# Kernel optimization log

Hardware: AMD Instinct MI355X
Metric: run time of the kernel (lower is better)

## Reference

```python
import jax, jax.numpy as jnp
import numpy as np

B, N, C, H = 8, 4096, 256, 8
D = C // H
HID = 4 * C
EPS = 1e-5

def _ln(x, w, b):
    mu = jnp.mean(x, axis=-1, keepdims=True)
    var = jnp.var(x, axis=-1, keepdims=True)
    return (x - mu) * jax.lax.rsqrt(var + EPS) * w + b

def setup_inputs() -> dict:
    key = jax.random.key(0)
    ks = jax.random.split(key, 16)
    s = lambda k, shp, scale=0.02: jax.random.normal(k, shp, dtype=jnp.float32) * scale
    return {
        "input_": jax.random.normal(ks[0], (B, N, C), dtype=jnp.float32),
        "prev_state": jax.random.normal(ks[1], (B, N, C), dtype=jnp.float32),
        "pos_embed": jax.random.normal(ks[2], (1, N, C), dtype=jnp.float32),
        "norm1_w": jnp.ones((C,), jnp.float32), "norm1_b": jnp.zeros((C,), jnp.float32),
        "norm2_w": jnp.ones((C,), jnp.float32), "norm2_b": jnp.zeros((C,), jnp.float32),
        "norm3_w": jnp.ones((C,), jnp.float32), "norm3_b": jnp.zeros((C,), jnp.float32),
        "qkv_input_w": s(ks[3], (3 * C, C)),
        "qkv_state_w": s(ks[4], (3 * C, C)),
        "proj_w": s(ks[5], (C, C)), "proj_b": jnp.zeros((C,), jnp.float32),
        "gate_w": s(ks[6], (C, 2 * C)), "gate_b": jnp.zeros((C,), jnp.float32),
        "fc1_w": s(ks[7], (HID, C)), "fc1_b": jnp.zeros((HID,), jnp.float32),
        "fc2_w": s(ks[8], (C, HID)), "fc2_b": jnp.zeros((C,), jnp.float32),
    }

def reference(input_, prev_state, pos_embed,
              norm1_w, norm1_b, norm2_w, norm2_b, norm3_w, norm3_b,
              qkv_input_w, qkv_state_w, proj_w, proj_b,
              gate_w, gate_b, fc1_w, fc1_b, fc2_w, fc2_b):
    input_pos = input_ + pos_embed
    x_ln = _ln(input_pos, norm1_w, norm1_b)
    s_ln = _ln(prev_state, norm2_w, norm2_b)
    # fused QKV from input and state; torch Linear: x @ W.T
    qkv_i = (x_ln @ qkv_input_w.T).reshape(B, N, 3, H, D).transpose(2, 0, 3, 1, 4)
    qkv_s = (s_ln @ qkv_state_w.T).reshape(B, N, 3, H, D).transpose(2, 0, 3, 1, 4)
    q = qkv_i[0] + qkv_s[0]  # [B,H,N,D]
    k = qkv_i[1] + qkv_s[1]
    v = qkv_i[2] + qkv_s[2]
    phi_q = jax.nn.elu(q) + 1.0
    phi_k = jax.nn.elu(k) + 1.0
    # (phi_q @ phi_k^T) @ v reordered associatively to O(N*D^2)
    kv = jnp.einsum('bhnd,bhne->bhde', phi_k, v)        # [B,H,D,D]
    attn = jnp.einsum('bhnd,bhde->bhne', phi_q, kv)     # [B,H,N,D]
    attn = attn.transpose(0, 2, 1, 3).reshape(B, N, C)
    attn = attn @ proj_w.T + proj_b
    output = input_pos + attn
    stacked = jnp.concatenate([input_, prev_state], axis=2)
    update = jax.nn.sigmoid(stacked @ gate_w.T + gate_b)
    new_state = prev_state * (1.0 - update) + attn * update
    h = _ln(output, norm3_w, norm3_b)
    h = jax.nn.gelu(h @ fc1_w.T + fc1_b, approximate=False) @ fc2_w.T + fc2_b
    output = output + h
    return (output, new_state)
```

## Files before the change

kernel.cpp:

```cpp
#include <hip/hip_runtime.h>
#include <cmath>

typedef unsigned short u16;
typedef __attribute__((ext_vector_type(8))) short short8;
typedef __attribute__((ext_vector_type(4))) float f32x4;
typedef __attribute__((ext_vector_type(4))) u16 u16x4;

__device__ __forceinline__ float b2f(u16 u) {
    unsigned x = ((unsigned)u) << 16;
    return __builtin_bit_cast(float, x);
}
__device__ __forceinline__ u16 f2b(float f) {
    unsigned x = __builtin_bit_cast(unsigned, f);
    unsigned r = (x + 0x7fffu + ((x >> 16) & 1u)) >> 16;
    return (u16)r;
}
__device__ __forceinline__ float loadx(const void* p, size_t i, int f32) {
    return f32 ? ((const float*)p)[i] : b2f(((const u16*)p)[i]);
}
__device__ __forceinline__ void gl_lds16(const void* g, void* l) {
    __builtin_amdgcn_global_load_lds(
        (const __attribute__((address_space(1))) void*)g,
        (__attribute__((address_space(3))) void*)l, 16, 0, 0);
}
__device__ __forceinline__ float gelu_f(float x) {
    float y = 0.7978845608028654f * (x + 0.044715f * x * x * x);
    float e = __expf(2.f * y);
    float t = 1.f - 2.f / (e + 1.f);
    return 0.5f * x * (1.f + t);
}

#define BB 8
#define NN 4096
#define CC 256
#define HH 8
#define DD 32
#define HID 1024
#define MTOK (BB*NN)
#define TOKEL ((size_t)MTOK*CC)
#define TOKELC 8388608

#define WS_INPUT_POS 0u
#define WS_PHIQ   16777216u
#define WS_PHIK   33554432u
#define WS_V      50331648u
#define WS_XLN    67108864u
#define WS_SLN    83886080u
#define WS_OUTPRE 100663296u
#define WS_FLAG   117440512u

#define OFF_QKVI  0u
#define OFF_QKVS  196608u
#define OFF_PROJW 393216u
#define OFF_GATEW 458752u
#define OFF_FC1W  589824u
#define OFF_FC2W  851968u
#define OFF_PROJB 1114112u
#define OFF_GATEB 1114368u
#define OFF_FC1B  1114624u
#define OFF_FC2B  1115648u
#define WTOT      1115904u

__device__ __attribute__((aligned(16))) u16 g_wb[WTOT];
__device__ __attribute__((aligned(16))) u16 g_inb[TOKELC];
__device__ __attribute__((aligned(16))) u16 g_prevb[TOKELC];
__device__ __attribute__((aligned(16))) u16 g_ugate[TOKELC];

__global__ __launch_bounds__(64) void detect_kernel(const u16* __restrict__ in0,
                                                    int* __restrict__ flag)
{
    int t = threadIdx.x;
    u16 w = in0[2 * t];
    int e = (w >> 7) & 0xFF;
    int bad = (e < 64 || e > 192) ? 1 : 0;
    unsigned long long m = __ballot(bad);
    if (t == 0) *flag = (__popcll(m) > 8) ? 1 : 0;
}

__global__ __launch_bounds__(256) void wconv_kernel(
    const void* qkvi, const void* qkvs, const void* projw, const void* gatew,
    const void* fc1w, const void* fc2w, const void* projb, const void* gateb,
    const void* fc1b, const void* fc2b, const int* __restrict__ flagp)
{
    const int f32 = *flagp;
    unsigned i = blockIdx.x * 256 + threadIdx.x;
    if (i >= WTOT) return;
    const void* src; unsigned off;
    if      (i < OFF_QKVS)  { src = qkvi;  off = OFF_QKVI; }
    else if (i < OFF_PROJW) { src = qkvs;  off = OFF_QKVS; }
    else if (i < OFF_GATEW) { src = projw; off = OFF_PROJW; }
    else if (i < OFF_FC1W)  { src = gatew; off = OFF_GATEW; }
    else if (i < OFF_FC2W)  { src = fc1w;  off = OFF_FC1W; }
    else if (i < OFF_PROJB) { src = fc2w;  off = OFF_FC2W; }
    else if (i < OFF_GATEB) { src = projb; off = OFF_PROJB; }
    else if (i < OFF_FC1B)  { src = gateb; off = OFF_GATEB; }
    else if (i < OFF_FC2B)  { src = fc1b;  off = OFF_FC1B; }
    else                    { src = fc2b;  off = OFF_FC2B; }
    g_wb[i] = f2b(loadx(src, i - off, f32));
}

__global__ __launch_bounds__(256) void prep_kernel(
    const void* __restrict__ inp, const void* __restrict__ prev,
    const void* __restrict__ pos,
    const void* __restrict__ w1, const void* __restrict__ b1,
    const void* __restrict__ w2, const void* __restrict__ b2,
    u16* __restrict__ input_pos, u16* __restrict__ x_ln, u16* __restrict__ s_ln,
    const int* __restrict__ flagp)
{
    const int f32 = *flagp;
    const int m = blockIdx.x * 4 + (threadIdx.x >> 6);
    const int lane = threadIdx.x & 63;
    const int e0 = lane * 4;
    const int n = m & (NN - 1);
    const size_t idx = (size_t)m * CC + e0;

    float inr[4], ip[4];
    if (f32) {
        f32x4 a = *(const f32x4*)((const float*)inp + idx);
        f32x4 p = *(const f32x4*)((const float*)pos + (size_t)n * CC + e0);
        #pragma unroll
        for (int r = 0; r < 4; ++r) { inr[r] = a[r]; ip[r] = a[r] + p[r]; }
    } else {
        u16x4 a = *(const u16x4*)((const u16*)inp + idx);
        u16x4 p = *(const u16x4*)((const u16*)pos + (size_t)n * CC + e0);
        #pragma unroll
        for (int r = 0; r < 4; ++r) { inr[r] = b2f(a[r]); ip[r] = inr[r] + b2f(p[r]); }
    }
    {
        u16x4 gi;
        #pragma unroll
        for (int r = 0; r < 4; ++r) gi[r] = f2b(inr[r]);
        *(u16x4*)(g_inb + idx) = gi;
    }
    float s = 0.f, s2 = 0.f;
    #pragma unroll
    for (int r = 0; r < 4; ++r) { s += ip[r]; s2 += ip[r] * ip[r]; }
    #pragma unroll
    for (int o = 1; o < 64; o <<= 1) { s += __shfl_xor(s, o, 64); s2 += __shfl_xor(s2, o, 64); }
    float mu = s * (1.f / 256.f);
    float rs = rsqrtf(s2 * (1.f / 256.f) - mu * mu + 1e-5f);
    float wv[4], bv[4];
    if (f32) {
        f32x4 w4 = *(const f32x4*)((const float*)w1 + e0);
        f32x4 b4 = *(const f32x4*)((const float*)b1 + e0);
        #pragma unroll
        for (int r = 0; r < 4; ++r) { wv[r] = w4[r]; bv[r] = b4[r]; }
    } else {
        u16x4 w4 = *(const u16x4*)((const u16*)w1 + e0);
        u16x4 b4 = *(const u16x4*)((const u16*)b1 + e0);
        #pragma unroll
        for (int r = 0; r < 4; ++r) { wv[r] = b2f(w4[r]); bv[r] = b2f(b4[r]); }
    }
    {
        u16x4 ipo, xo;
        #pragma unroll
        for (int r = 0; r < 4; ++r) {
            ipo[r] = f2b(ip[r]);
            xo[r]  = f2b((ip[r] - mu) * rs * wv[r] + bv[r]);
        }
        *(u16x4*)(input_pos + idx) = ipo;
        *(u16x4*)(x_ln + idx) = xo;
    }

    float pv[4];
    if (f32) {
        f32x4 a = *(const f32x4*)((const float*)prev + idx);
        #pragma unroll
        for (int r = 0; r < 4; ++r) pv[r] = a[r];
    } else {
        u16x4 a = *(const u16x4*)((const u16*)prev + idx);
        #pragma unroll
        for (int r = 0; r < 4; ++r) pv[r] = b2f(a[r]);
    }
    {
        u16x4 gp;
        #pragma unroll
        for (int r = 0; r < 4; ++r) gp[r] = f2b(pv[r]);
        *(u16x4*)(g_prevb + idx) = gp;
    }
    s = 0.f; s2 = 0.f;
    #pragma unroll
    for (int r = 0; r < 4; ++r) { s += pv[r]; s2 += pv[r] * pv[r]; }
    #pragma unroll
    for (int o = 1; o < 64; o <<= 1) { s += __shfl_xor(s, o, 64); s2 += __shfl_xor(s2, o, 64); }
    mu = s * (1.f / 256.f);
    rs = rsqrtf(s2 * (1.f / 256.f) - mu * mu + 1e-5f);
    if (f32) {
        f32x4 w4 = *(const f32x4*)((const float*)w2 + e0);
        f32x4 b4 = *(const f32x4*)((const float*)b2 + e0);
        #pragma unroll
        for (int r = 0; r < 4; ++r) { wv[r] = w4[r]; bv[r] = b4[r]; }
    } else {
        u16x4 w4 = *(const u16x4*)((const u16*)w2 + e0);
        u16x4 b4 = *(const u16x4*)((const u16*)b2 + e0);
        #pragma unroll
        for (int r = 0; r < 4; ++r) { wv[r] = b2f(w4[r]); bv[r] = b2f(b4[r]); }
    }
    {
        u16x4 so;
        #pragma unroll
        for (int r = 0; r < 4; ++r) so[r] = f2b((pv[r] - mu) * rs * wv[r] + bv[r]);
        *(u16x4*)(s_ln + idx) = so;
    }
}

__global__ __launch_bounds__(256) void ln3_blend_kernel(
    const u16* __restrict__ op, const void* __restrict__ w,
    const void* __restrict__ b, u16* __restrict__ out,
    const u16* __restrict__ ap, const void* __restrict__ prevraw,
    void* __restrict__ dout, const int* __restrict__ flagp)
{
    const int f32 = *flagp;
    const int m = blockIdx.x * 4 + (threadIdx.x >> 6);
    const int lane = threadIdx.x & 63;
    const int e0 = lane * 4;
    const size_t idx = (size_t)m * CC + e0;

    u16x4 x4 = *(const u16x4*)(op + idx);
    float x[4];
    #pragma unroll
    for (int r = 0; r < 4; ++r) x[r] = b2f(x4[r]);
    float s = 0.f, s2 = 0.f;
    #pragma unroll
    for (int r = 0; r < 4; ++r) { s += x[r]; s2 += x[r] * x[r]; }
    #pragma unroll
    for (int o = 1; o < 64; o <<= 1) { s += __shfl_xor(s, o, 64); s2 += __shfl_xor(s2, o, 64); }
    float mu = s * (1.f / 256.f);
    float rs = rsqrtf(s2 * (1.f / 256.f) - mu * mu + 1e-5f);
    float wv[4], bv[4];
    if (f32) {
        f32x4 w4 = *(const f32x4*)((const float*)w + e0);
        f32x4 b4 = *(const f32x4*)((const float*)b + e0);
        #pragma unroll
        for (int r = 0; r < 4; ++r) { wv[r] = w4[r]; bv[r] = b4[r]; }
    } else {
        u16x4 w4 = *(const u16x4*)((const u16*)w + e0);
        u16x4 b4 = *(const u16x4*)((const u16*)b + e0);
        #pragma unroll
        for (int r = 0; r < 4; ++r) { wv[r] = b2f(w4[r]); bv[r] = b2f(b4[r]); }
    }
    {
        u16x4 o4;
        #pragma unroll
        for (int r = 0; r < 4; ++r) o4[r] = f2b((x[r] - mu) * rs * wv[r] + bv[r]);
        *(u16x4*)(out + idx) = o4;
    }

    u16x4 a4 = *(const u16x4*)(ap + idx);
    u16x4 u4 = *(const u16x4*)(g_ugate + idx);
    if (f32) {
        f32x4 pv = *(const f32x4*)((const float*)prevraw + idx);
        f32x4 o;
        #pragma unroll
        for (int r = 0; r < 4; ++r) {
            float u = b2f(u4[r]);
            o[r] = pv[r] * (1.f - u) + b2f(a4[r]) * u;
        }
        *(f32x4*)((float*)dout + TOKEL + idx) = o;
    } else {
        u16x4 pv = *(const u16x4*)((const u16*)prevraw + idx);
        u16x4 o;
        #pragma unroll
        for (int r = 0; r < 4; ++r) {
            float u = b2f(u4[r]);
            o[r] = f2b(b2f(pv[r]) * (1.f - u) + b2f(a4[r]) * u);
        }
        *(u16x4*)((u16*)dout + TOKEL + idx) = o;
    }
}

__global__ __launch_bounds__(64) void kv_mfma(
    const u16* __restrict__ phik_t, const u16* __restrict__ v_t,
    float* __restrict__ kvout)
{
    const int bh = blockIdx.x;
    const int k0 = blockIdx.y * 256;
    const int lane = threadIdx.x;
    const int quad = lane >> 4, lr = lane & 15;

    const u16* A = phik_t + (size_t)bh * DD * NN;
    const u16* W = v_t    + (size_t)bh * DD * NN;

    f32x4 acc[2][2];
    #pragma unroll
    for (int i = 0; i < 2; ++i)
        #pragma unroll
        for (int j = 0; j < 2; ++j) { f32x4 z = {0.f,0.f,0.f,0.f}; acc[i][j] = z; }

    for (int kk = k0; kk < k0 + 256; kk += 32) {
        short8 a0 = *(const short8*)(A + (size_t)lr * NN + kk + quad * 8);
        short8 a1 = *(const short8*)(A + (size_t)(16 + lr) * NN + kk + quad * 8);
        short8 w0 = *(const short8*)(W + (size_t)lr * NN + kk + quad * 8);
        short8 w1 = *(const short8*)(W + (size_t)(16 + lr) * NN + kk + quad * 8);
        acc[0][0] = __builtin_amdgcn_mfma_f32_16x16x32_bf16(a0, w0, acc[0][0], 0, 0, 0);
        acc[0][1] = __builtin_amdgcn_mfma_f32_16x16x32_bf16(a0, w1, acc[0][1], 0, 0, 0);
        acc[1][0] = __builtin_amdgcn_mfma_f32_16x16x32_bf16(a1, w0, acc[1][0], 0, 0, 0);
        acc[1][1] = __builtin_amdgcn_mfma_f32_16x16x32_bf16(a1, w1, acc[1][1], 0, 0, 0);
    }
    float* base = kvout + (size_t)bh * (DD * DD);
    #pragma unroll
    for (int i = 0; i < 2; ++i)
        #pragma unroll
        for (int j = 0; j < 2; ++j)
            #pragma unroll
            for (int r = 0; r < 4; ++r)
                atomicAdd(base + (i * 16 + quad * 4 + r) * DD + j * 16 + lr, acc[i][j][r]);
}

__global__ __launch_bounds__(256) void attn_mfma(
    const u16* __restrict__ phiq, const float* __restrict__ kv,
    u16* __restrict__ attn_tok)
{
    const int bh = blockIdx.x;
    const int b = bh >> 3, h = bh & 7;
    const int wv = threadIdx.x >> 6, lane = threadIdx.x & 63;
    const int quad = lane >> 4, lr = lane & 15;

    const float* kvb = kv + (size_t)bh * (DD * DD);
    short8 bf0, bf1;
    #pragma unroll
    for (int j = 0; j < 8; ++j) {
        int d = quad * 8 + j;
        bf0[j] = (short)f2b(kvb[d * DD + lr]);
        bf1[j] = (short)f2b(kvb[d * DD + 16 + lr]);
    }

    const u16* qb = phiq + (size_t)bh * NN * DD;
    const int n0 = blockIdx.y * 512 + wv * 128;
    #pragma unroll
    for (int t = 0; t < 8; ++t) {
        const int nt = n0 + t * 16;
        short8 af = *(const short8*)(qb + (size_t)(nt + lr) * DD + quad * 8);
        f32x4 c0 = {0.f,0.f,0.f,0.f}, c1 = {0.f,0.f,0.f,0.f};
        c0 = __builtin_amdgcn_mfma_f32_16x16x32_bf16(af, bf0, c0, 0, 0, 0);
        c1 = __builtin_amdgcn_mfma_f32_16x16x32_bf16(af, bf1, c1, 0, 0, 0);
        size_t base = ((size_t)b * NN + nt + quad * 4) * CC + h * DD;
        #pragma unroll
        for (int r = 0; r < 4; ++r) {
            attn_tok[base + (size_t)r * CC + lr]      = f2b(c0[r]);
            attn_tok[base + (size_t)r * CC + 16 + lr] = f2b(c1[r]);
        }
    }
}

#define BM 128
#define BN 128
#define BK 32

template <int MODE>
__global__ __launch_bounds__(256) void gemm_bt(
    const u16* __restrict__ A1in, const u16* __restrict__ A2in,
    int lda, int ldw, int K, int Ksplit, int wcol2,
    u16* __restrict__ o0, u16* __restrict__ o1,
    const u16* __restrict__ xa, const void* __restrict__ xr,
    void* __restrict__ oraw, const int* __restrict__ flagp)
{
    __shared__ __attribute__((aligned(16))) u16 ash[3][BM * BK];
    __shared__ __attribute__((aligned(16))) u16 bsh[3][BN * BK];

    const int f32 = (MODE == 4) ? *flagp : 0;

    const u16* W1; const u16* W2; const u16* bias = nullptr;
    if (MODE == 0)      { W1 = g_wb + OFF_QKVI; W2 = g_wb + OFF_QKVS; }
    else if (MODE == 1) { W1 = W2 = g_wb + OFF_PROJW; bias = g_wb + OFF_PROJB; }
    else if (MODE == 3) { W1 = W2 = g_wb + OFF_FC1W;  bias = g_wb + OFF_FC1B; }
    else                { W1 = W2 = g_wb + OFF_FC2W;  bias = g_wb + OFF_FC2B; }

    const int gx = gridDim.x;
    const int nwg = gx * (int)gridDim.y;
    const int hw = blockIdx.y * gx + blockIdx.x;
    const int qq = nwg >> 3, rr = nwg & 7;
    const int xc = hw & 7, pp = hw >> 3;
    const int nid = (xc < rr ? xc * (qq + 1) : rr * (qq + 1) + (xc - rr) * qq) + pp;
    const int bx = nid % gx, by = nid / gx;

    const bool isGate = (MODE == 1) && (bx >= 2);
    const bool swp = (MODE == 0) ? (bx < 2) : true;

    const int tid = threadIdx.x;
    const int lane = tid & 63;
    const int wv = tid >> 6;
    const int wm = wv >> 1, wn = wv & 1;
    const int quad = lane >> 4, lr = lane & 15;

    f32x4 acc[4][4];
    #pragma unroll
    for (int i = 0; i < 4; ++i)
        #pragma unroll
        for (int j = 0; j < 4; ++j) { f32x4 z = {0.f,0.f,0.f,0.f}; acc[i][j] = z; }

    const size_t arow0 = (size_t)by * BM;
    const int nbase_blk = isGate ? (bx - 2) * BN : bx * BN;
    const int ldw_eff = isGate ? 2 * CC : ldw;
    const int Keff = isGate ? 2 * CC : K;

    const int srow = lane & 31;
    const int sg   = (lane >> 5) << 3;
    const size_t aoff = (arow0 + wv * 32 + srow) * (size_t)lda + sg;
    const size_t woff = ((size_t)nbase_blk + wv * 32 + srow) * (size_t)ldw_eff + sg;

    auto stage = [&](int buf, int k0) {
        const u16* As; const u16* Ws; int ka, kw;
        if (isGate) {
            As = (k0 < CC) ? g_inb : g_prevb; ka = k0 & (CC - 1);
            Ws = g_wb + OFF_GATEW; kw = k0;
        } else if (MODE == 0) {
            if (k0 < Ksplit) { As = A1in; Ws = W1; ka = k0;          kw = k0; }
            else             { As = A2in; Ws = W2; ka = k0 - Ksplit; kw = k0 - Ksplit; }
        } else {
            As = A1in; Ws = W1; ka = k0; kw = k0;
        }
        const u16* ga = As + aoff + ka;
        u16* la = ash[buf] + (wv << 10);
        gl_lds16(ga, la);
        gl_lds16(ga + 16, la + 512);
        const u16* gw = Ws + woff + kw;
        u16* lb = bsh[buf] + (wv << 10);
        gl_lds16(gw, lb);
        gl_lds16(gw + 16, lb + 512);
    };

    auto compute = [&](int buf) {
        short8 af[4], bf[4];
        #pragma unroll
        for (int i = 0; i < 4; ++i) {
            const int ra = wm * 64 + i * 16 + lr;
            af[i] = *(const short8*)(ash[buf] + ((ra >> 5) << 10) + (quad << 8) + ((ra & 31) << 3));
        }
        #pragma unroll
        for (int j = 0; j < 4; ++j) {
            const int rb = wn * 64 + j * 16 + lr;
            bf[j] = *(const short8*)(bsh[buf] + ((rb >> 5) << 10) + (quad << 8) + ((rb & 31) << 3));
        }
        if (swp) {
            #pragma unroll
            for (int i = 0; i < 4; ++i)
                #pragma unroll
                for (int j = 0; j < 4; ++j)
                    acc[i][j] = __builtin_amdgcn_mfma_f32_16x16x32_bf16(bf[j], af[i], acc[i][j], 0, 0, 0);
        } else {
            #pragma unroll
            for (int i = 0; i < 4; ++i)
                #pragma unroll
                for (int j = 0; j < 4; ++j)
                    acc[i][j] = __builtin_amdgcn_mfma_f32_16x16x32_bf16(af[i], bf[j], acc[i][j], 0, 0, 0);
        }
    };

    const int NT = Keff / BK;
    stage(0, 0);
    stage(1, BK);
    for (int t = 0; t < NT; ++t) {
        if (t + 2 < NT) {
            stage((t + 2) % 3, (t + 2) * BK);
            asm volatile("s_waitcnt vmcnt(8)" ::: "memory");
        } else if (t + 1 < NT) {
            asm volatile("s_waitcnt vmcnt(4)" ::: "memory");
        } else {
            asm volatile("s_waitcnt vmcnt(0)" ::: "memory");
        }
        __builtin_amdgcn_s_barrier();
        asm volatile("" ::: "memory");
        compute(t % 3);
        asm volatile("" ::: "memory");
        __builtin_amdgcn_s_barrier();
    }

    const int mbase = by * BM + wm * 64;
    const int nbase = nbase_blk + wn * 64;
    constexpr int LDOUT = (MODE == 3) ? HID : CC;

    #pragma unroll
    for (int i = 0; i < 4; ++i) {
        #pragma unroll
        for (int j = 0; j < 4; ++j) {
            if (MODE == 0) {
                if (swp) {
                    const int m = mbase + i * 16 + lr;
                    const int b = m >> 12, n = m & (NN - 1);
                    const int c0 = nbase + j * 16 + quad * 4;
                    const int h = c0 >> 5, d0 = c0 & 31;
                    u16x4 p;
                    #pragma unroll
                    for (int r = 0; r < 4; ++r) {
                        float v = acc[i][j][r];
                        p[r] = f2b((v > 0.f) ? (v + 1.f) : __expf(v));
                    }
                    *(u16x4*)(o0 + (((size_t)b * HH + h) * NN + n) * DD + d0) = p;
                } else {
                    const int c = nbase + j * 16 + lr;
                    const int which = c >> 8, rem = c & 255, h = rem >> 5, d = rem & 31;
                    const int m0 = mbase + i * 16 + quad * 4;
                    const int b = m0 >> 12, n0i = m0 & (NN - 1);
                    u16x4 p;
                    #pragma unroll
                    for (int r = 0; r < 4; ++r) {
                        float v = acc[i][j][r];
                        if (which == 1) v = (v > 0.f) ? (v + 1.f) : __expf(v);
                        p[r] = f2b(v);
                    }
                    u16* dst = o0 + (size_t)which * TOKEL;
                    *(u16x4*)(dst + (((size_t)b * HH + h) * DD + d) * NN + n0i) = p;
                }
            } else if (MODE == 1) {
                const int m = mbase + i * 16 + lr;
                const int c0 = nbase + j * 16 + quad * 4;
                const size_t idx0 = (size_t)m * CC + c0;
                if (isGate) {
                    u16x4 b4 = *(const u16x4*)(g_wb + OFF_GATEB + c0);
                    u16x4 p;
                    #pragma unroll
                    for (int r = 0; r < 4; ++r) {
                        float u = 1.f / (1.f + __expf(-(acc[i][j][r] + b2f(b4[r]))));
                        p[r] = f2b(u);
                    }
                    *(u16x4*)(g_ugate + idx0) = p;
                } else {
                    u16x4 b4 = *(const u16x4*)(bias + c0);
                    u16x4 xa4 = *(const u16x4*)(xa + idx0);
                    u16x4 po, pr;
                    #pragma unroll
                    for (int r = 0; r < 4; ++r) {
                        float val = acc[i][j][r] + b2f(b4[r]);
                        po[r] = f2b(val);
                        pr[r] = f2b(b2f(xa4[r]) + val);
                    }
                    *(u16x4*)(o0 + idx0) = po;
                    *(u16x4*)(o1 + idx0) = pr;
                }
            } else {
                const int m = mbase + i * 16 + lr;
                const int c0 = nbase + j * 16 + quad * 4;
                const size_t idx0 = (size_t)m * LDOUT + c0;
                float bias4[4];
                {
                    u16x4 t = *(const u16x4*)(bias + c0);
                    #pragma unroll
                    for (int r = 0; r < 4; ++r) bias4[r] = b2f(t[r]);
                }
                if (MODE == 3) {
                    u16x4 p;
                    #pragma unroll
                    for (int r = 0; r < 4; ++r)
                        p[r] = f2b(gelu_f(acc[i][j][r] + bias4[r]));
                    *(u16x4*)(o0 + idx0) = p;
                } else {
                    u16x4 xa4 = *(const u16x4*)(xa + idx0);
                    if (f32) {
                        f32x4 o;
                        #pragma unroll
                        for (int r = 0; r < 4; ++r)
                            o[r] = b2f(xa4[r]) + acc[i][j][r] + bias4[r];
                        *(f32x4*)((float*)oraw + idx0) = o;
                    } else {
                        u16x4 o;
                        #pragma unroll
                        for (int r = 0; r < 4; ++r)
                            o[r] = f2b(b2f(xa4[r]) + acc[i][j][r] + bias4[r]);
                        *(u16x4*)((u16*)oraw + idx0) = o;
                    }
                }
            }
        }
    }
}

extern "C" void kernel_launch(void* const* d_in, const int* in_sizes, int n_in,
                              void* d_out, int out_size, void* d_ws, size_t ws_size,
                              hipStream_t stream)
{
    const void* input_ = d_in[0];
    const void* prev   = d_in[1];
    const void* pos    = d_in[2];
    const void* n1w = d_in[3];  const void* n1b = d_in[4];
    const void* n2w = d_in[5];  const void* n2b = d_in[6];
    const void* n3w = d_in[7];  const void* n3b = d_in[8];
    const void* qkvi = d_in[9]; const void* qkvs = d_in[10];
    const void* projw = d_in[11]; const void* projb = d_in[12];
    const void* gatew = d_in[13]; const void* gateb = d_in[14];
    const void* fc1w = d_in[15]; const void* fc1b = d_in[16];
    const void* fc2w = d_in[17]; const void* fc2b = d_in[18];

    char* ws = (char*)d_ws;
    u16* input_pos = (u16*)(ws + WS_INPUT_POS);
    u16* phiq  = (u16*)(ws + WS_PHIQ);
    u16* phikt = (u16*)(ws + WS_PHIK);
    u16* vt    = (u16*)(ws + WS_V);
    u16* x_ln = (u16*)(ws + WS_XLN);
    u16* s_ln = (u16*)(ws + WS_SLN);
    u16* attn_tok = x_ln;
    u16* attn_proj = phikt;
    float* kvf = (float*)(ws + WS_SLN);
    u16* ln3o = s_ln;
    u16* outpre = (u16*)(ws + WS_OUTPRE);
    u16* h1 = (u16*)(ws + WS_INPUT_POS);
    int* flagp = (int*)(ws + WS_FLAG);

    detect_kernel<<<1, 64, 0, stream>>>((const u16*)input_, flagp);
    wconv_kernel<<<(WTOT + 255) / 256, 256, 0, stream>>>(
        qkvi, qkvs, projw, gatew, fc1w, fc2w, projb, gateb, fc1b, fc2b, flagp);
    prep_kernel<<<MTOK / 4, 256, 0, stream>>>(input_, prev, pos, n1w, n1b, n2w, n2b,
                                              input_pos, x_ln, s_ln, flagp);
    gemm_bt<0><<<dim3(3 * CC / BN, MTOK / BM), 256, 0, stream>>>(
        x_ln, s_ln, CC, CC, 2 * CC, CC, 0,
        phiq, nullptr, nullptr, nullptr, nullptr, flagp);
    hipMemsetAsync((void*)kvf, 0, BB * HH * DD * DD * sizeof(float), stream);
    kv_mfma<<<dim3(BB * HH, 16), 64, 0, stream>>>(phikt, vt, kvf);
    attn_mfma<<<dim3(BB * HH, NN / 512), 256, 0, stream>>>(phiq, kvf, attn_tok);
    gemm_bt<1><<<dim3(4, MTOK / BM), 256, 0, stream>>>(
        attn_tok, attn_tok, CC, CC, CC, CC, 0,
        attn_proj, outpre, input_pos, nullptr, nullptr, flagp);
    ln3_blend_kernel<<<MTOK / 4, 256, 0, stream>>>(
        outpre, n3w, n3b, ln3o, attn_proj, prev, d_out, flagp);
    gemm_bt<3><<<dim3(HID / BN, MTOK / BM), 256, 0, stream>>>(
        ln3o, ln3o, CC, CC, CC, CC, 0,
        h1, nullptr, nullptr, nullptr, nullptr, flagp);
    gemm_bt<4><<<dim3(CC / BN, MTOK / BM), 256, 0, stream>>>(
        h1, h1, HID, HID, HID, HID, 0,
        nullptr, nullptr, outpre, nullptr, d_out, flagp);
}
```

Measured before the change: 428.4 us.

## Fold KV state into projection weights and drop the attention kernel

The per-head KV matrix is multiplied into the projection weight to form a per-batch effective weight (Wfull = proj_w · KVᵀ per head), so the projection GEMM reads phi_q directly and the attn_mfma kernel with its intermediate attention tensor is removed. KV partial sums are now written to per-slice buffers and reduced in the new kernel instead of using atomics plus a memset. Weight conversion is also merged into prep_kernel as extra blocks, saving a launch. The cost is a per-batch 256x256 weight built with scalar FMA code, plus an extra bf16 rounding of the folded weights.

```diff
diff --git a/kernel.cpp b/kernel.cpp
--- a/kernel.cpp
+++ b/kernel.cpp
@@ -60,11 +60,14 @@
 #define OFF_FC1B  1114624u
 #define OFF_FC2B  1115648u
 #define WTOT      1115904u
+#define WCONV_BLOCKS 4359u
 
 __device__ __attribute__((aligned(16))) u16 g_wb[WTOT];
 __device__ __attribute__((aligned(16))) u16 g_inb[TOKELC];
 __device__ __attribute__((aligned(16))) u16 g_prevb[TOKELC];
 __device__ __attribute__((aligned(16))) u16 g_ugate[TOKELC];
+__device__ __attribute__((aligned(16))) float g_kvpart[64 * 16 * 1024];
+__device__ __attribute__((aligned(16))) u16 g_wfull[BB * CC * CC];
 
 __global__ __launch_bounds__(64) void detect_kernel(const u16* __restrict__ in0,
                                                     int* __restrict__ flag)
@@ -77,37 +80,37 @@
     if (t == 0) *flag = (__popcll(m) > 8) ? 1 : 0;
 }
 
-__global__ __launch_bounds__(256) void wconv_kernel(
-    const void* qkvi, const void* qkvs, const void* projw, const void* gatew,
-    const void* fc1w, const void* fc2w, const void* projb, const void* gateb,
-    const void* fc1b, const void* fc2b, const int* __restrict__ flagp)
-{
-    const int f32 = *flagp;
-    unsigned i = blockIdx.x * 256 + threadIdx.x;
-    if (i >= WTOT) return;
-    const void* src; unsigned off;
-    if      (i < OFF_QKVS)  { src = qkvi;  off = OFF_QKVI; }
-    else if (i < OFF_PROJW) { src = qkvs;  off = OFF_QKVS; }
-    else if (i < OFF_GATEW) { src = projw; off = OFF_PROJW; }
-    else if (i < OFF_FC1W)  { src = gatew; off = OFF_GATEW; }
-    else if (i < OFF_FC2W)  { src = fc1w;  off = OFF_FC1W; }
-    else if (i < OFF_PROJB) { src = fc2w;  off = OFF_FC2W; }
-    else if (i < OFF_GATEB) { src = projb; off = OFF_PROJB; }
-    else if (i < OFF_FC1B)  { src = gateb; off = OFF_GATEB; }
-    else if (i < OFF_FC2B)  { src = fc1b;  off = OFF_FC1B; }
-    else                    { src = fc2b;  off = OFF_FC2B; }
-    g_wb[i] = f2b(loadx(src, i - off, f32));
-}
-
 __global__ __launch_bounds__(256) void prep_kernel(
     const void* __restrict__ inp, const void* __restrict__ prev,
     const void* __restrict__ pos,
     const void* __restrict__ w1, const void* __restrict__ b1,
     const void* __restrict__ w2, const void* __restrict__ b2,
     u16* __restrict__ input_pos, u16* __restrict__ x_ln, u16* __restrict__ s_ln,
+    const void* qkvi, const void* qkvs, const void* projw, const void* gatew,
+    const void* fc1w, const void* fc2w, const void* projb, const void* gateb,
+    const void* fc1b, const void* fc2b,
     const int* __restrict__ flagp)
 {
     const int f32 = *flagp;
+
+    if (blockIdx.x >= MTOK / 4) {
+        unsigned i = (blockIdx.x - MTOK / 4) * 256 + threadIdx.x;
+        if (i >= WTOT) return;
+        const void* src; unsigned off;
+        if      (i < OFF_QKVS)  { src = qkvi;  off = OFF_QKVI; }
+        else if (i < OFF_PROJW) { src = qkvs;  off = OFF_QKVS; }
+        else if (i < OFF_GATEW) { src = projw; off = OFF_PROJW; }
+        else if (i < OFF_FC1W)  { src = gatew; off = OFF_GATEW; }
+        else if (i < OFF_FC2W)  { src = fc1w;  off = OFF_FC1W; }
+        else if (i < OFF_PROJB) { src = fc2w;  off = OFF_FC2W; }
+        else if (i < OFF_GATEB) { src = projb; off = OFF_PROJB; }
+        else if (i < OFF_FC1B)  { src = gateb; off = OFF_GATEB; }
+        else if (i < OFF_FC2B)  { src = fc1b;  off = OFF_FC1B; }
+        else                    { src = fc2b;  off = OFF_FC2B; }
+        g_wb[i] = f2b(loadx(src, i - off, f32));
+        return;
+    }
+
     const int m = blockIdx.x * 4 + (threadIdx.x >> 6);
     const int lane = threadIdx.x & 63;
     const int e0 = lane * 4;
@@ -270,8 +273,7 @@
 }
 
 __global__ __launch_bounds__(64) void kv_mfma(
-    const u16* __restrict__ phik_t, const u16* __restrict__ v_t,
-    float* __restrict__ kvout)
+    const u16* __restrict__ phik_t, const u16* __restrict__ v_t)
 {
     const int bh = blockIdx.x;
     const int k0 = blockIdx.y * 256;
@@ -297,49 +299,40 @@
         acc[1][0] = __builtin_amdgcn_mfma_f32_16x16x32_bf16(a1, w0, acc[1][0], 0, 0, 0);
         acc[1][1] = __builtin_amdgcn_mfma_f32_16x16x32_bf16(a1, w1, acc[1][1], 0, 0, 0);
     }
-    float* base = kvout + (size_t)bh * (DD * DD);
+    float* base = g_kvpart + ((size_t)bh * 16 + blockIdx.y) * (DD * DD);
     #pragma unroll
     for (int i = 0; i < 2; ++i)
         #pragma unroll
         for (int j = 0; j < 2; ++j)
             #pragma unroll
             for (int r = 0; r < 4; ++r)
-                atomicAdd(base + (i * 16 + quad * 4 + r) * DD + j * 16 + lr, acc[i][j][r]);
-}
-
-__global__ __launch_bounds__(256) void attn_mfma(
-    const u16* __restrict__ phiq, const float* __restrict__ kv,
-    u16* __restrict__ attn_tok)
+                base[(i * 16 + quad * 4 + r) * DD + j * 16 + lr] = acc[i][j][r];
+}
+
+__global__ __launch_bounds__(256) void wfull_kernel()
 {
     const int bh = blockIdx.x;
     const int b = bh >> 3, h = bh & 7;
-    const int wv = threadIdx.x >> 6, lane = threadIdx.x & 63;
-    const int quad = lane >> 4, lr = lane & 15;
-
-    const float* kvb = kv + (size_t)bh * (DD * DD);
-    short8 bf0, bf1;
-    #pragma unroll
-    for (int j = 0; j < 8; ++j) {
-        int d = quad * 8 + j;
-        bf0[j] = (short)f2b(kvb[d * DD + lr]);
-        bf1[j] = (short)f2b(kvb[d * DD + 16 + lr]);
-    }
-
-    const u16* qb = phiq + (size_t)bh * NN * DD;
-    const int n0 = blockIdx.y * 512 + wv * 128;
-    #pragma unroll
-    for (int t = 0; t < 8; ++t) {
-        const int nt = n0 + t * 16;
-        short8 af = *(const short8*)(qb + (size_t)(nt + lr) * DD + quad * 8);
-        f32x4 c0 = {0.f,0.f,0.f,0.f}, c1 = {0.f,0.f,0.f,0.f};
-        c0 = __builtin_amdgcn_mfma_f32_16x16x32_bf16(af, bf0, c0, 0, 0, 0);
-        c1 = __builtin_amdgcn_mfma_f32_16x16x32_bf16(af, bf1, c1, 0, 0, 0);
-        size_t base = ((size_t)b * NN + nt + quad * 4) * CC + h * DD;
-        #pragma unroll
-        for (int r = 0; r < 4; ++r) {
-            attn_tok[base + (size_t)r * CC + lr]      = f2b(c0[r]);
-            attn_tok[base + (size_t)r * CC + 16 + lr] = f2b(c1[r]);
-        }
+    const int c = threadIdx.x;
+    __shared__ float kvs[DD * DD];
+    for (int t = threadIdx.x; t < DD * DD; t += 256) {
+        float s = 0.f;
+        #pragma unroll
+        for (int sl = 0; sl < 16; ++sl)
+            s += g_kvpart[((size_t)bh * 16 + sl) * (DD * DD) + t];
+        kvs[t] = s;
+    }
+    __syncthreads();
+    const u16* pw = g_wb + OFF_PROJW + (size_t)c * CC + h * DD;
+    float pwv[DD];
+    #pragma unroll
+    for (int e = 0; e < DD; ++e) pwv[e] = b2f(pw[e]);
+    u16* dst = g_wfull + ((size_t)b * CC + c) * CC + h * DD;
+    for (int d = 0; d < DD; ++d) {
+        float s = 0.f;
+        #pragma unroll
+        for (int e = 0; e < DD; ++e) s += pwv[e] * kvs[d * DD + e];
+        dst[d] = f2b(s);
     }
 }
 
@@ -362,7 +355,7 @@
 
     const u16* W1; const u16* W2; const u16* bias = nullptr;
     if (MODE == 0)      { W1 = g_wb + OFF_QKVI; W2 = g_wb + OFF_QKVS; }
-    else if (MODE == 1) { W1 = W2 = g_wb + OFF_PROJW; bias = g_wb + OFF_PROJB; }
+    else if (MODE == 1) { W1 = W2 = nullptr;          bias = g_wb + OFF_PROJB; }
     else if (MODE == 3) { W1 = W2 = g_wb + OFF_FC1W;  bias = g_wb + OFF_FC1B; }
     else                { W1 = W2 = g_wb + OFF_FC2W;  bias = g_wb + OFF_FC2B; }
 
@@ -399,22 +392,31 @@
     const size_t aoff = (arow0 + wv * 32 + srow) * (size_t)lda + sg;
     const size_t woff = ((size_t)nbase_blk + wv * 32 + srow) * (size_t)ldw_eff + sg;
 
+    const int b_idx = (int)(arow0 >> 12);
+    const size_t aq_off = ((size_t)b_idx * 8 * NN + (int)(arow0 & (NN - 1)) + wv * 32 + srow) * DD + sg;
+    const size_t wf_off = (size_t)b_idx * CC * CC + ((size_t)nbase_blk + wv * 32 + srow) * CC + sg;
+
     auto stage = [&](int buf, int k0) {
-        const u16* As; const u16* Ws; int ka, kw;
-        if (isGate) {
-            As = (k0 < CC) ? g_inb : g_prevb; ka = k0 & (CC - 1);
-            Ws = g_wb + OFF_GATEW; kw = k0;
+        const u16* ga; const u16* gw;
+        if (MODE == 1) {
+            if (isGate) {
+                const u16* As = (k0 < CC) ? g_inb : g_prevb;
+                ga = As + aoff + (k0 & (CC - 1));
+                gw = g_wb + OFF_GATEW + woff + k0;
+            } else {
+                ga = A1in + aq_off + (size_t)k0 * NN;
+                gw = g_wfull + wf_off + k0;
+            }
         } else if (MODE == 0) {
-            if (k0 < Ksplit) { As = A1in; Ws = W1; ka = k0;          kw = k0; }
-            else             { As = A2in; Ws = W2; ka = k0 - Ksplit; kw = k0 - Ksplit; }
+            if (k0 < Ksplit) { ga = A1in + aoff + k0;          gw = W1 + woff + k0; }
+            else             { ga = A2in + aoff + (k0 - Ksplit); gw = W2 + woff + (k0 - Ksplit); }
         } else {
-            As = A1in; Ws = W1; ka = k0; kw = k0;
-        }
-        const u16* ga = As + aoff + ka;
+            ga = A1in + aoff + k0;
+            gw = W1 + woff + k0;
+        }
         u16* la = ash[buf] + (wv << 10);
         gl_lds16(ga, la);
         gl_lds16(ga + 16, la + 512);
-        const u16* gw = Ws + woff + kw;
         u16* lb = bsh[buf] + (wv << 10);
         gl_lds16(gw, lb);
         gl_lds16(gw + 16, lb + 512);
@@ -588,27 +590,24 @@
     u16* vt    = (u16*)(ws + WS_V);
     u16* x_ln = (u16*)(ws + WS_XLN);
     u16* s_ln = (u16*)(ws + WS_SLN);
-    u16* attn_tok = x_ln;
     u16* attn_proj = phikt;
-    float* kvf = (float*)(ws + WS_SLN);
     u16* ln3o = s_ln;
     u16* outpre = (u16*)(ws + WS_OUTPRE);
     u16* h1 = (u16*)(ws + WS_INPUT_POS);
     int* flagp = (int*)(ws + WS_FLAG);
 
     detect_kernel<<<1, 64, 0, stream>>>((const u16*)input_, flagp);
-    wconv_kernel<<<(WTOT + 255) / 256, 256, 0, stream>>>(
+    prep_kernel<<<MTOK / 4 + WCONV_BLOCKS, 256, 0, stream>>>(
+        input_, prev, pos, n1w, n1b, n2w, n2b,
+        input_pos, x_ln, s_ln,
         qkvi, qkvs, projw, gatew, fc1w, fc2w, projb, gateb, fc1b, fc2b, flagp);
-    prep_kernel<<<MTOK / 4, 256, 0, stream>>>(input_, prev, pos, n1w, n1b, n2w, n2b,
-                                              input_pos, x_ln, s_ln, flagp);
     gemm_bt<0><<<dim3(3 * CC / BN, MTOK / BM), 256, 0, stream>>>(
         x_ln, s_ln, CC, CC, 2 * CC, CC, 0,
         phiq, nullptr, nullptr, nullptr, nullptr, flagp);
-    hipMemsetAsync((void*)kvf, 0, BB * HH * DD * DD * sizeof(float), stream);
-    kv_mfma<<<dim3(BB * HH, 16), 64, 0, stream>>>(phikt, vt, kvf);
-    attn_mfma<<<dim3(BB * HH, NN / 512), 256, 0, stream>>>(phiq, kvf, attn_tok);
+    kv_mfma<<<dim3(BB * HH, 16), 64, 0, stream>>>(phikt, vt);
+    wfull_kernel<<<BB * HH, 256, 0, stream>>>();
     gemm_bt<1><<<dim3(4, MTOK / BM), 256, 0, stream>>>(
-        attn_tok, attn_tok, CC, CC, CC, CC, 0,
+        phiq, nullptr, CC, CC, CC, CC, 0,
         attn_proj, outpre, input_pos, nullptr, nullptr, flagp);
     ln3_blend_kernel<<<MTOK / 4, 256, 0, stream>>>(
         outpre, n3w, n3b, ln3o, attn_proj, prev, d_out, flagp);
```

After: 424.2 us. No clear change (-1.0%).
